# Kernel optimization log

Hardware: AMD Instinct MI355X
Metric: run time of the kernel (lower is better)

Reference implementation:

```python
import jax, jax.numpy as jnp
import numpy as np

N = 50000      # num_nodes
E = 800000     # num_edges (avg degree 16)
F_IN = 128     # num_features
H = 64         # hidden dim (fixed in module code)
C = 16         # num_classes
R = 8          # num_relations
BN_EPS = 1e-5


def setup_inputs() -> dict:
    key = jax.random.key(0)
    ks = jax.random.split(key, 16)
    s = 0.05
    f32 = jnp.float32
    inp = {
        "x": jax.random.normal(ks[0], (N, F_IN), f32),
        "edge_index": jax.random.randint(ks[1], (2, E), 0, N, dtype=jnp.int32),
        "edge_type": jax.random.randint(ks[2], (E,), 0, R, dtype=jnp.int32),
        # RGCNConv layer 1: per-relation weights, root weight, bias
        "W1": jax.random.normal(ks[3], (R, F_IN, H), f32) * s,
        "root1": jax.random.normal(ks[4], (F_IN, H), f32) * s,
        "b1": jnp.zeros((H,), f32),
        # RGCNConv layer 2
        "W2": jax.random.normal(ks[5], (R, H, H), f32) * s,
        "root2": jax.random.normal(ks[6], (H, H), f32) * s,
        "b2": jnp.zeros((H,), f32),
        # RGCNConv layer 3
        "W3": jax.random.normal(ks[7], (R, H, H), f32) * s,
        "root3": jax.random.normal(ks[8], (H, H), f32) * s,
        "b3": jnp.zeros((H,), f32),
        # BatchNorm1d params + running stats (eval mode)
        "gamma1": jnp.ones((H,), f32), "beta1": jnp.zeros((H,), f32),
        "rm1": jnp.zeros((H,), f32),   "rv1": jnp.ones((H,), f32),
        "gamma2": jnp.ones((H,), f32), "beta2": jnp.zeros((H,), f32),
        "rm2": jnp.zeros((H,), f32),   "rv2": jnp.ones((H,), f32),
        "gamma3": jnp.ones((H,), f32), "beta3": jnp.zeros((H,), f32),
        "rm3": jnp.zeros((H,), f32),   "rv3": jnp.ones((H,), f32),
        # final linear
        "Wl": jax.random.normal(ks[9], (H, C), f32) * s,
        "bl": jnp.zeros((C,), f32),
    }
    return inp


def _rgcn(x, src, dst, edge_type, W, root, bias):
    # RGCNConv with mean aggregation per relation (PyG default):
    # out_i = x_i @ root + bias + sum_r mean_{j in N_r(i)} (x_j @ W_r)
    out = x @ root + bias
    for r in range(R):  # small fixed loop over relations
        h = x @ W[r]                      # [N, H] node-level transform
        mask = (edge_type == r)
        msg = jnp.where(mask[:, None], h[src], 0.0)   # [E, H]
        agg = jax.ops.segment_sum(msg, dst, num_segments=N)   # [N, H]
        cnt = jax.ops.segment_sum(mask.astype(x.dtype), dst, num_segments=N)
        out = out + agg / jnp.maximum(cnt, 1.0)[:, None]
    return out


def _bn(x, gamma, beta, rm, rv):
    # BatchNorm1d in eval mode with running stats
    return (x - rm) * jax.lax.rsqrt(rv + BN_EPS) * gamma + beta


def reference(x, edge_index, edge_type,
              W1, root1, b1, W2, root2, b2, W3, root3, b3,
              gamma1, beta1, rm1, rv1,
              gamma2, beta2, rm2, rv2,
              gamma3, beta3, rm3, rv3,
              Wl, bl):
    src, dst = edge_index[0], edge_index[1]
    h = jax.nn.relu(_rgcn(x, src, dst, edge_type, W1, root1, b1))
    h = _bn(h, gamma1, beta1, rm1, rv1)  # dropout = identity in eval
    h = jax.nn.relu(_rgcn(h, src, dst, edge_type, W2, root2, b2))
    h = _bn(h, gamma2, beta2, rm2, rv2)
    h = jax.nn.relu(_rgcn(h, src, dst, edge_type, W3, root3, b3))
    h = _bn(h, gamma3, beta3, rm3, rv3)
    return h @ Wl + bl  # [N, C]
```

## Files before the change

kernel.cpp:

```cpp
#include <hip/hip_runtime.h>


#define R_REL 8

typedef unsigned short ushort_t;
typedef short short8 __attribute__((ext_vector_type(8)));
typedef float f32x4 __attribute__((ext_vector_type(4)));

#define MFMA(a, b, c) __builtin_amdgcn_mfma_f32_16x16x32_bf16(a, b, c, 0, 0, 0)

static __device__ __forceinline__ unsigned short f2bf(float f) {
    unsigned int u = __float_as_uint(f);
    u = (u + 0x7FFF + ((u >> 16) & 1)) >> 16;
    return (unsigned short)u;
}
static __device__ __forceinline__ float bf2f(unsigned short h) {
    return __uint_as_float(((unsigned int)h) << 16);
}

struct WcvtA {
    const float* src[6];
    ushort_t*    dst[6];
    int          end[6];
    int          K[6];
};
__global__ void wcvt6_kernel(WcvtA a, int total)
{
    int i = blockIdx.x * 256 + threadIdx.x;
    if (i >= total) return;
    int s = 0;
    while (i >= a.end[s]) ++s;
    int j = i - (s ? a.end[s - 1] : 0);
    int K = a.K[s];
    int g = j / (K * 64), rem = j % (K * 64), k = rem >> 6, c = rem & 63;
    a.dst[s][(size_t)g * 64 * K + (size_t)c * K + k] = f2bf(a.src[s][j]);
}

template<int K, bool AF32>
__global__ __launch_bounds__(256)
void mgemm_kernel(const void* __restrict__ Av, int n,
                  const ushort_t* __restrict__ WT, const ushort_t* __restrict__ RT,
                  const float* __restrict__ bias,
                  ushort_t* __restrict__ H, float* __restrict__ accb)
{
    __shared__ ushort_t As[64][136];
    __shared__ ushort_t Bs[64][136];

    const int row0 = blockIdx.x * 64;
    const int yr = blockIdx.y;
    const ushort_t* Bsrc = (yr < R_REL) ? (WT + (size_t)yr * 64 * K) : RT;

    const int tid = threadIdx.x;
    const int KB = K >> 3;

    for (int i = tid; i < 64 * KB; i += 256) {
        int r = i / KB, k8 = (i % KB) << 3;
        *(uint4*)&Bs[r][k8] = *(const uint4*)&Bsrc[(size_t)r * K + k8];
        if (AF32) {
            const float* Af = (const float*)Av;
            float4 f0 = make_float4(0.f, 0.f, 0.f, 0.f), f1 = f0;
            if (row0 + r < n) {
                f0 = *(const float4*)&Af[(size_t)(row0 + r) * K + k8];
                f1 = *(const float4*)&Af[(size_t)(row0 + r) * K + k8 + 4];
            }
            ushort_t t[8] = {f2bf(f0.x), f2bf(f0.y), f2bf(f0.z), f2bf(f0.w),
                             f2bf(f1.x), f2bf(f1.y), f2bf(f1.z), f2bf(f1.w)};
            *(uint4*)&As[r][k8] = *(const uint4*)t;
        } else {
            const ushort_t* Ab = (const ushort_t*)Av;
            uint4 av = make_uint4(0u, 0u, 0u, 0u);
            if (row0 + r < n) av = *(const uint4*)&Ab[(size_t)(row0 + r) * K + k8];
            *(uint4*)&As[r][k8] = av;
        }
    }
    __syncthreads();

    const int wid  = tid >> 6;
    const int lane = tid & 63;
    const int wr = (wid >> 1) << 5;
    const int wc = (wid & 1) << 5;
    const int fr = lane & 15;
    const int kg = (lane >> 4) << 3;

    f32x4 acc[2][2] = {};
    #pragma unroll
    for (int k0 = 0; k0 < K; k0 += 32) {
        short8 a0 = *(const short8*)&As[wr + fr     ][k0 + kg];
        short8 a1 = *(const short8*)&As[wr + 16 + fr][k0 + kg];
        short8 b0 = *(const short8*)&Bs[wc + fr     ][k0 + kg];
        short8 b1 = *(const short8*)&Bs[wc + 16 + fr][k0 + kg];
        acc[0][0] = MFMA(a0, b0, acc[0][0]);
        acc[0][1] = MFMA(a0, b1, acc[0][1]);
        acc[1][0] = MFMA(a1, b0, acc[1][0]);
        acc[1][1] = MFMA(a1, b1, acc[1][1]);
    }
    __syncthreads();

    float* Ct = (float*)As;
    const int rbase = (lane >> 4) << 2;
    #pragma unroll
    for (int m = 0; m < 2; ++m)
        #pragma unroll
        for (int nn = 0; nn < 2; ++nn)
            #pragma unroll
            for (int j = 0; j < 4; ++j)
                Ct[(wr + m * 16 + rbase + j) * 68 + wc + nn * 16 + fr] = acc[m][nn][j];
    __syncthreads();

    if (yr < R_REL) {
        const int cb = yr << 6;
        for (int i = tid; i < 64 * 8; i += 256) {
            int r = i >> 3, c8 = (i & 7) << 3;
            if (row0 + r < n) {
                ushort_t t[8];
                #pragma unroll
                for (int j = 0; j < 8; ++j) t[j] = f2bf(Ct[r * 68 + c8 + j]);
                *(uint4*)&H[(size_t)(row0 + r) * 512 + cb + c8] = *(const uint4*)t;
            }
        }
    } else {
        for (int i = tid; i < 64 * 16; i += 256) {
            int r = i >> 4, c4 = (i & 15) << 2;
            if (row0 + r < n) {
                float4 o;
                o.x = Ct[r * 68 + c4 + 0] + bias[c4 + 0];
                o.y = Ct[r * 68 + c4 + 1] + bias[c4 + 1];
                o.z = Ct[r * 68 + c4 + 2] + bias[c4 + 2];
                o.w = Ct[r * 68 + c4 + 3] + bias[c4 + 3];
                *(float4*)&accb[(size_t)(row0 + r) * 64 + c4] = o;
            }
        }
    }
}

__global__ void count_kernel(const int* __restrict__ ei, const int* __restrict__ et,
                             int* __restrict__ cnt, int E)
{
    int e = blockIdx.x * 256 + threadIdx.x;
    if (e < E) atomicAdd(&cnt[(size_t)ei[E + e] * R_REL + et[e]], 1);
}

__global__ void invdeg_scan_kernel(float* __restrict__ inv, int* __restrict__ deg,
                                   int* __restrict__ offs, int* __restrict__ partials,
                                   int N)
{
    __shared__ int sm[256];
    int i = blockIdx.x * 256 + threadIdx.x;
    int tot = 0;
    if (i < N) {
        const int* c = (const int*)inv;
        float out[R_REL];
        #pragma unroll
        for (int r = 0; r < R_REL; ++r) {
            int cc = c[(size_t)i * R_REL + r];
            tot += cc;
            out[r] = 1.0f / (float)(cc > 1 ? cc : 1);
        }
        #pragma unroll
        for (int r = 0; r < R_REL; ++r) inv[(size_t)i * R_REL + r] = out[r];
        deg[i] = tot;
    }
    sm[threadIdx.x] = tot;
    __syncthreads();
    for (int off = 1; off < 256; off <<= 1) {
        int t = (threadIdx.x >= off) ? sm[threadIdx.x - off] : 0;
        __syncthreads();
        sm[threadIdx.x] += t;
        __syncthreads();
    }
    if (i < N) offs[i] = sm[threadIdx.x] - tot;
    if (threadIdx.x == 255) partials[blockIdx.x] = sm[255];
}

__global__ void scan2_kernel(int* __restrict__ partials, int P)
{
    __shared__ int sm[256];
    __shared__ int carry;
    if (threadIdx.x == 0) carry = 0;
    __syncthreads();
    for (int base = 0; base < P; base += 256) {
        int i = base + threadIdx.x;
        int c = (i < P) ? partials[i] : 0;
        sm[threadIdx.x] = c;
        __syncthreads();
        for (int off = 1; off < 256; off <<= 1) {
            int t = (threadIdx.x >= off) ? sm[threadIdx.x - off] : 0;
            __syncthreads();
            sm[threadIdx.x] += t;
            __syncthreads();
        }
        int incl = sm[threadIdx.x];
        int cold = carry;
        if (i < P) partials[i] = incl - c + cold;
        __syncthreads();
        if (threadIdx.x == 0) carry = cold + sm[255];
        __syncthreads();
    }
}

__global__ void scan3_kernel(int* __restrict__ offs, const int* __restrict__ partials, int N)
{
    int i = blockIdx.x * 256 + threadIdx.x;
    if (i < N) offs[i] += partials[blockIdx.x];
}

__global__ void fill3_kernel(const int* __restrict__ ei, const int* __restrict__ et,
                             const int* __restrict__ offs, int* __restrict__ cursor,
                             const float* __restrict__ inv,
                             int2* __restrict__ ep, int E)
{
    int e = blockIdx.x * 256 + threadIdx.x;
    if (e >= E) return;
    int d = ei[E + e];
    int r = et[e];
    int pos = offs[d] + atomicAdd(&cursor[d], 1);
    ep[pos] = make_int2(ei[e] * 512 + r * 64,
                        __float_as_int(inv[(size_t)d * R_REL + r]));
}

__global__ __launch_bounds__(256)
void agg5_kernel(const int2* __restrict__ ep,
                 const int* __restrict__ offs, const int* __restrict__ deg,
                 const ushort_t* __restrict__ H, const float* __restrict__ accb,
                 const float* __restrict__ g, const float* __restrict__ b,
                 const float* __restrict__ rm, const float* __restrict__ rv,
                 ushort_t* __restrict__ xout,
                 const float* __restrict__ Wl, const float* __restrict__ bl,
                 float* __restrict__ out, int N, int last)
{
    const int lane = threadIdx.x & 63;
    const int d = (blockIdx.x * 256 + threadIdx.x) >> 6;
    if (d >= N) return;

    const int sub = lane >> 4;
    const int fl  = lane & 15;
    const int n0 = offs[d];
    const int dg = deg[d];

    float s0 = 0.f, s1 = 0.f, s2 = 0.f, s3 = 0.f;
    int k = 0;

    for (; k + 8 <= dg; k += 8) {
        int2 eA = ep[n0 + k + sub];
        int2 eB = ep[n0 + k + 4 + sub];
        uint2 hA = *(const uint2*)&H[(size_t)eA.x + (fl << 2)];
        uint2 hB = *(const uint2*)&H[(size_t)eB.x + (fl << 2)];
        float wA = __int_as_float(eA.y);
        float wB = __int_as_float(eB.y);
        s0 += bf2f((ushort_t)(hA.x & 0xFFFF)) * wA + bf2f((ushort_t)(hB.x & 0xFFFF)) * wB;
        s1 += bf2f((ushort_t)(hA.x >> 16))    * wA + bf2f((ushort_t)(hB.x >> 16))    * wB;
        s2 += bf2f((ushort_t)(hA.y & 0xFFFF)) * wA + bf2f((ushort_t)(hB.y & 0xFFFF)) * wB;
        s3 += bf2f((ushort_t)(hA.y >> 16))    * wA + bf2f((ushort_t)(hB.y >> 16))    * wB;
    }
    for (; k + 4 <= dg; k += 4) {
        int2 eA = ep[n0 + k + sub];
        uint2 hA = *(const uint2*)&H[(size_t)eA.x + (fl << 2)];
        float wA = __int_as_float(eA.y);
        s0 += bf2f((ushort_t)(hA.x & 0xFFFF)) * wA;
        s1 += bf2f((ushort_t)(hA.x >> 16))    * wA;
        s2 += bf2f((ushort_t)(hA.y & 0xFFFF)) * wA;
        s3 += bf2f((ushort_t)(hA.y >> 16))    * wA;
    }
    if (k < dg && sub < dg - k) {
        int2 eA = ep[n0 + k + sub];
        uint2 hA = *(const uint2*)&H[(size_t)eA.x + (fl << 2)];
        float wA = __int_as_float(eA.y);
        s0 += bf2f((ushort_t)(hA.x & 0xFFFF)) * wA;
        s1 += bf2f((ushort_t)(hA.x >> 16))    * wA;
        s2 += bf2f((ushort_t)(hA.y & 0xFFFF)) * wA;
        s3 += bf2f((ushort_t)(hA.y >> 16))    * wA;
    }

    s0 += __shfl_xor(s0, 16); s1 += __shfl_xor(s1, 16);
    s2 += __shfl_xor(s2, 16); s3 += __shfl_xor(s3, 16);
    s0 += __shfl_xor(s0, 32); s1 += __shfl_xor(s1, 32);
    s2 += __shfl_xor(s2, 32); s3 += __shfl_xor(s3, 32);

    if (sub == 0) {
        const int c4 = fl << 2;
        float4 aq = *(const float4*)&accb[(size_t)d * 64 + c4];
        float4 gm = *(const float4*)&g[c4];
        float4 bt = *(const float4*)&b[c4];
        float4 mu = *(const float4*)&rm[c4];
        float4 vr = *(const float4*)&rv[c4];
        float t0 = aq.x + s0, t1 = aq.y + s1, t2 = aq.z + s2, t3 = aq.w + s3;
        t0 = t0 > 0.f ? t0 : 0.f;  t1 = t1 > 0.f ? t1 : 0.f;
        t2 = t2 > 0.f ? t2 : 0.f;  t3 = t3 > 0.f ? t3 : 0.f;
        t0 = (t0 - mu.x) * rsqrtf(vr.x + 1e-5f) * gm.x + bt.x;
        t1 = (t1 - mu.y) * rsqrtf(vr.y + 1e-5f) * gm.y + bt.y;
        t2 = (t2 - mu.z) * rsqrtf(vr.z + 1e-5f) * gm.z + bt.z;
        t3 = (t3 - mu.w) * rsqrtf(vr.w + 1e-5f) * gm.w + bt.w;

        if (!last) {
            ushort_t o[4] = {f2bf(t0), f2bf(t1), f2bf(t2), f2bf(t3)};
            *(uint2*)&xout[(size_t)d * 64 + c4] = *(const uint2*)o;
        } else {
            f32x4 p[4] = {};
            float tt[4] = {t0, t1, t2, t3};
            #pragma unroll
            for (int i = 0; i < 4; ++i) {
                const float* wrow = &Wl[(size_t)(c4 + i) * 16];
                #pragma unroll
                for (int q = 0; q < 4; ++q)
                    p[q] += tt[i] * (*(const f32x4*)&wrow[q * 4]);
            }
            #pragma unroll
            for (int m = 1; m < 16; m <<= 1) {
                #pragma unroll
                for (int q = 0; q < 4; ++q) {
                    p[q][0] += __shfl_xor(p[q][0], m);
                    p[q][1] += __shfl_xor(p[q][1], m);
                    p[q][2] += __shfl_xor(p[q][2], m);
                    p[q][3] += __shfl_xor(p[q][3], m);
                }
            }
            if (fl == 0) {
                #pragma unroll
                for (int q = 0; q < 4; ++q) {
                    f32x4 bv = *(const f32x4*)&bl[q * 4];
                    f32x4 o = p[q] + bv;
                    *(f32x4*)&out[(size_t)d * 16 + q * 4] = o;
                }
            }
        }
    }
}

extern "C" void kernel_launch(void* const* d_in, const int* in_sizes, int n_in,
                              void* d_out, int out_size, void* d_ws, size_t ws_size,
                              hipStream_t stream)
{
    const float* x  = (const float*)d_in[0];
    const int*   ei = (const int*)d_in[1];
    const int*   et = (const int*)d_in[2];
    const float* W[3]    = {(const float*)d_in[3], (const float*)d_in[6], (const float*)d_in[9]};
    const float* root[3] = {(const float*)d_in[4], (const float*)d_in[7], (const float*)d_in[10]};
    const float* bias[3] = {(const float*)d_in[5], (const float*)d_in[8], (const float*)d_in[11]};
    const float* gamma[3] = {(const float*)d_in[12], (const float*)d_in[16], (const float*)d_in[20]};
    const float* beta[3]  = {(const float*)d_in[13], (const float*)d_in[17], (const float*)d_in[21]};
    const float* rm[3]    = {(const float*)d_in[14], (const float*)d_in[18], (const float*)d_in[22]};
    const float* rv[3]    = {(const float*)d_in[15], (const float*)d_in[19], (const float*)d_in[23]};
    const float* Wl = (const float*)d_in[24];
    const float* bl = (const float*)d_in[25];

    const int N = in_sizes[0] / 128;
    const int E = in_sizes[2];
    const int K1 = 128;

    char* p = (char*)d_ws;
    float*   inv  = (float*)p;    p += (size_t)N * R_REL * 4;
    ushort_t* Hbuf = (ushort_t*)p; p += (size_t)N * 512 * 2;
    float*   accb = (float*)p;    p += (size_t)N * 64 * 4;
    ushort_t* xb  = (ushort_t*)p; p += (size_t)N * 64 * 2;
    ushort_t* wt0 = (ushort_t*)p; p += (size_t)R_REL * 64 * K1 * 2;
    ushort_t* wt1 = (ushort_t*)p; p += (size_t)R_REL * 64 * 64 * 2;
    ushort_t* wt2 = (ushort_t*)p; p += (size_t)R_REL * 64 * 64 * 2;
    ushort_t* rt0 = (ushort_t*)p; p += (size_t)64 * K1 * 2;
    ushort_t* rt1 = (ushort_t*)p; p += (size_t)64 * 64 * 2;
    ushort_t* rt2 = (ushort_t*)p; p += (size_t)64 * 64 * 2;
    int*   offs    = (int*)p;     p += (size_t)N * 4;
    int*   deg     = (int*)p;     p += (size_t)N * 4;
    int*   cursor  = (int*)p;     p += (size_t)N * 4;
    int2*  ep      = (int2*)p;    p += (size_t)E * 8;
    int*   partials = (int*)p;

    const ushort_t* wt[3] = {wt0, wt1, wt2};
    const ushort_t* rt[3] = {rt0, rt1, rt2};

    const int gxN = (N + 255) / 256;

    {
        WcvtA a;
        a.src[0] = W[0];   a.dst[0] = wt0; a.K[0] = K1;
        a.src[1] = W[1];   a.dst[1] = wt1; a.K[1] = 64;
        a.src[2] = W[2];   a.dst[2] = wt2; a.K[2] = 64;
        a.src[3] = root[0]; a.dst[3] = rt0; a.K[3] = K1;
        a.src[4] = root[1]; a.dst[4] = rt1; a.K[4] = 64;
        a.src[5] = root[2]; a.dst[5] = rt2; a.K[5] = 64;
        int sizes[6] = {R_REL * K1 * 64, R_REL * 64 * 64, R_REL * 64 * 64,
                        K1 * 64, 64 * 64, 64 * 64};
        int acc = 0;
        for (int i = 0; i < 6; ++i) { acc += sizes[i]; a.end[i] = acc; }
        wcvt6_kernel<<<(acc + 255) / 256, 256, 0, stream>>>(a, acc);
    }

    hipMemsetAsync(inv, 0, (size_t)N * R_REL * 4, stream);
    hipMemsetAsync(cursor, 0, (size_t)N * 4, stream);
    count_kernel<<<(E + 255) / 256, 256, 0, stream>>>(ei, et, (int*)inv, E);
    invdeg_scan_kernel<<<gxN, 256, 0, stream>>>(inv, deg, offs, partials, N);
    scan2_kernel<<<1, 256, 0, stream>>>(partials, gxN);
    scan3_kernel<<<gxN, 256, 0, stream>>>(offs, partials, N);
    fill3_kernel<<<(E + 255) / 256, 256, 0, stream>>>(ei, et, offs, cursor, inv, ep, E);

    const int gx = (N + 63) / 64;
    const int gagg = (N * 64 + 255) / 256;
    const ushort_t* cur = nullptr;
    for (int layer = 0; layer < 3; ++layer) {
        if (layer == 0)
            mgemm_kernel<128, true><<<dim3(gx, R_REL + 1), 256, 0, stream>>>(
                (const void*)x, N, wt[0], rt[0], bias[0], Hbuf, accb);
        else
            mgemm_kernel<64, false><<<dim3(gx, R_REL + 1), 256, 0, stream>>>(
                (const void*)cur, N, wt[layer], rt[layer], bias[layer], Hbuf, accb);
        int last = (layer == 2);
        agg5_kernel<<<gagg, 256, 0, stream>>>(
            ep, offs, deg, Hbuf, accb,
            gamma[layer], beta[layer], rm[layer], rv[layer],
            xb, Wl, bl, (float*)d_out, N, last);
        cur = xb;
    }
}
```

Before: 413.3 us.

## Reuse A tile across three relation weights per GEMM block; split final linear

The GEMM now loads the activation tile into LDS once and loops over three weight matrices (relations or root) per block, so grid.y drops from 9 to 3 and A loads and the fp32-to-bf16 conversion are amortised. A separate C tile buffer is added in shared memory, which raises LDS use per block. The final BN-then-linear projection is moved out of the aggregation kernel into a separate lin_kernel that reads the bf16 layer output. This simplifies the aggregation kernel but adds a launch and an extra round trip of the last hidden layer through memory.

```diff
diff --git a/kernel.cpp b/kernel.cpp
--- a/kernel.cpp
+++ b/kernel.cpp
@@ -38,24 +38,21 @@
 
 template<int K, bool AF32>
 __global__ __launch_bounds__(256)
-void mgemm_kernel(const void* __restrict__ Av, int n,
-                  const ushort_t* __restrict__ WT, const ushort_t* __restrict__ RT,
-                  const float* __restrict__ bias,
-                  ushort_t* __restrict__ H, float* __restrict__ accb)
-{
-    __shared__ ushort_t As[64][136];
-    __shared__ ushort_t Bs[64][136];
+void mgemm3_kernel(const void* __restrict__ Av, int n,
+                   const ushort_t* __restrict__ WT, const ushort_t* __restrict__ RT,
+                   const float* __restrict__ bias,
+                   ushort_t* __restrict__ H, float* __restrict__ accb)
+{
+    __shared__ ushort_t As[64][K + 8];
+    __shared__ ushort_t Bs[64][K + 8];
+    __shared__ float    Ct[64][68];
 
     const int row0 = blockIdx.x * 64;
-    const int yr = blockIdx.y;
-    const ushort_t* Bsrc = (yr < R_REL) ? (WT + (size_t)yr * 64 * K) : RT;
-
     const int tid = threadIdx.x;
     const int KB = K >> 3;
 
     for (int i = tid; i < 64 * KB; i += 256) {
         int r = i / KB, k8 = (i % KB) << 3;
-        *(uint4*)&Bs[r][k8] = *(const uint4*)&Bsrc[(size_t)r * K + k8];
         if (AF32) {
             const float* Af = (const float*)Av;
             float4 f0 = make_float4(0.f, 0.f, 0.f, 0.f), f1 = f0;
@@ -73,7 +70,6 @@
             *(uint4*)&As[r][k8] = av;
         }
     }
-    __syncthreads();
 
     const int wid  = tid >> 6;
     const int lane = tid & 63;
@@ -81,53 +77,64 @@
     const int wc = (wid & 1) << 5;
     const int fr = lane & 15;
     const int kg = (lane >> 4) << 3;
-
-    f32x4 acc[2][2] = {};
-    #pragma unroll
-    for (int k0 = 0; k0 < K; k0 += 32) {
-        short8 a0 = *(const short8*)&As[wr + fr     ][k0 + kg];
-        short8 a1 = *(const short8*)&As[wr + 16 + fr][k0 + kg];
-        short8 b0 = *(const short8*)&Bs[wc + fr     ][k0 + kg];
-        short8 b1 = *(const short8*)&Bs[wc + 16 + fr][k0 + kg];
-        acc[0][0] = MFMA(a0, b0, acc[0][0]);
-        acc[0][1] = MFMA(a0, b1, acc[0][1]);
-        acc[1][0] = MFMA(a1, b0, acc[1][0]);
-        acc[1][1] = MFMA(a1, b1, acc[1][1]);
-    }
-    __syncthreads();
-
-    float* Ct = (float*)As;
     const int rbase = (lane >> 4) << 2;
-    #pragma unroll
-    for (int m = 0; m < 2; ++m)
+
+    for (int j = 0; j < 3; ++j) {
+        const int r = blockIdx.y * 3 + j;
+        const ushort_t* Bsrc = (r < R_REL) ? (WT + (size_t)r * 64 * K) : RT;
+
+        __syncthreads();
+        for (int i = tid; i < 64 * KB; i += 256) {
+            int rr = i / KB, k8 = (i % KB) << 3;
+            *(uint4*)&Bs[rr][k8] = *(const uint4*)&Bsrc[(size_t)rr * K + k8];
+        }
+        __syncthreads();
+
+        f32x4 acc[2][2] = {};
         #pragma unroll
-        for (int nn = 0; nn < 2; ++nn)
+        for (int k0 = 0; k0 < K; k0 += 32) {
+            short8 a0 = *(const short8*)&As[wr + fr     ][k0 + kg];
+            short8 a1 = *(const short8*)&As[wr + 16 + fr][k0 + kg];
+            short8 b0 = *(const short8*)&Bs[wc + fr     ][k0 + kg];
+            short8 b1 = *(const short8*)&Bs[wc + 16 + fr][k0 + kg];
+            acc[0][0] = MFMA(a0, b0, acc[0][0]);
+            acc[0][1] = MFMA(a0, b1, acc[0][1]);
+            acc[1][0] = MFMA(a1, b0, acc[1][0]);
+            acc[1][1] = MFMA(a1, b1, acc[1][1]);
+        }
+        __syncthreads();
+
+        #pragma unroll
+        for (int m = 0; m < 2; ++m)
             #pragma unroll
-            for (int j = 0; j < 4; ++j)
-                Ct[(wr + m * 16 + rbase + j) * 68 + wc + nn * 16 + fr] = acc[m][nn][j];
-    __syncthreads();
-
-    if (yr < R_REL) {
-        const int cb = yr << 6;
-        for (int i = tid; i < 64 * 8; i += 256) {
-            int r = i >> 3, c8 = (i & 7) << 3;
-            if (row0 + r < n) {
-                ushort_t t[8];
+            for (int nn = 0; nn < 2; ++nn)
                 #pragma unroll
-                for (int j = 0; j < 8; ++j) t[j] = f2bf(Ct[r * 68 + c8 + j]);
-                *(uint4*)&H[(size_t)(row0 + r) * 512 + cb + c8] = *(const uint4*)t;
+                for (int q = 0; q < 4; ++q)
+                    Ct[wr + m * 16 + rbase + q][wc + nn * 16 + fr] = acc[m][nn][q];
+        __syncthreads();
+
+        if (r < R_REL) {
+            const int cb = r << 6;
+            for (int i = tid; i < 64 * 8; i += 256) {
+                int rr = i >> 3, c8 = (i & 7) << 3;
+                if (row0 + rr < n) {
+                    ushort_t t[8];
+                    #pragma unroll
+                    for (int q = 0; q < 8; ++q) t[q] = f2bf(Ct[rr][c8 + q]);
+                    *(uint4*)&H[(size_t)(row0 + rr) * 512 + cb + c8] = *(const uint4*)t;
+                }
             }
-        }
-    } else {
-        for (int i = tid; i < 64 * 16; i += 256) {
-            int r = i >> 4, c4 = (i & 15) << 2;
-            if (row0 + r < n) {
-                float4 o;
-                o.x = Ct[r * 68 + c4 + 0] + bias[c4 + 0];
-                o.y = Ct[r * 68 + c4 + 1] + bias[c4 + 1];
-                o.z = Ct[r * 68 + c4 + 2] + bias[c4 + 2];
-                o.w = Ct[r * 68 + c4 + 3] + bias[c4 + 3];
-                *(float4*)&accb[(size_t)(row0 + r) * 64 + c4] = o;
+        } else {
+            for (int i = tid; i < 64 * 16; i += 256) {
+                int rr = i >> 4, c4 = (i & 15) << 2;
+                if (row0 + rr < n) {
+                    float4 o;
+                    o.x = Ct[rr][c4 + 0] + bias[c4 + 0];
+                    o.y = Ct[rr][c4 + 1] + bias[c4 + 1];
+                    o.z = Ct[rr][c4 + 2] + bias[c4 + 2];
+                    o.w = Ct[rr][c4 + 3] + bias[c4 + 3];
+                    *(float4*)&accb[(size_t)(row0 + rr) * 64 + c4] = o;
+                }
             }
         }
     }
@@ -219,14 +226,12 @@
 }
 
 __global__ __launch_bounds__(256)
-void agg5_kernel(const int2* __restrict__ ep,
+void agg3_kernel(const int2* __restrict__ ep,
                  const int* __restrict__ offs, const int* __restrict__ deg,
                  const ushort_t* __restrict__ H, const float* __restrict__ accb,
                  const float* __restrict__ g, const float* __restrict__ b,
                  const float* __restrict__ rm, const float* __restrict__ rv,
-                 ushort_t* __restrict__ xout,
-                 const float* __restrict__ Wl, const float* __restrict__ bl,
-                 float* __restrict__ out, int N, int last)
+                 ushort_t* __restrict__ xout, int N)
 {
     const int lane = threadIdx.x & 63;
     const int d = (blockIdx.x * 256 + threadIdx.x) >> 6;
@@ -278,52 +283,41 @@
 
     if (sub == 0) {
         const int c4 = fl << 2;
-        float4 aq = *(const float4*)&accb[(size_t)d * 64 + c4];
+        float4 a  = *(const float4*)&accb[(size_t)d * 64 + c4];
         float4 gm = *(const float4*)&g[c4];
         float4 bt = *(const float4*)&b[c4];
         float4 mu = *(const float4*)&rm[c4];
         float4 vr = *(const float4*)&rv[c4];
-        float t0 = aq.x + s0, t1 = aq.y + s1, t2 = aq.z + s2, t3 = aq.w + s3;
+        float t0 = a.x + s0, t1 = a.y + s1, t2 = a.z + s2, t3 = a.w + s3;
         t0 = t0 > 0.f ? t0 : 0.f;  t1 = t1 > 0.f ? t1 : 0.f;
         t2 = t2 > 0.f ? t2 : 0.f;  t3 = t3 > 0.f ? t3 : 0.f;
         t0 = (t0 - mu.x) * rsqrtf(vr.x + 1e-5f) * gm.x + bt.x;
         t1 = (t1 - mu.y) * rsqrtf(vr.y + 1e-5f) * gm.y + bt.y;
         t2 = (t2 - mu.z) * rsqrtf(vr.z + 1e-5f) * gm.z + bt.z;
         t3 = (t3 - mu.w) * rsqrtf(vr.w + 1e-5f) * gm.w + bt.w;
-
-        if (!last) {
-            ushort_t o[4] = {f2bf(t0), f2bf(t1), f2bf(t2), f2bf(t3)};
-            *(uint2*)&xout[(size_t)d * 64 + c4] = *(const uint2*)o;
-        } else {
-            f32x4 p[4] = {};
-            float tt[4] = {t0, t1, t2, t3};
-            #pragma unroll
-            for (int i = 0; i < 4; ++i) {
-                const float* wrow = &Wl[(size_t)(c4 + i) * 16];
-                #pragma unroll
-                for (int q = 0; q < 4; ++q)
-                    p[q] += tt[i] * (*(const f32x4*)&wrow[q * 4]);
-            }
-            #pragma unroll
-            for (int m = 1; m < 16; m <<= 1) {
-                #pragma unroll
-                for (int q = 0; q < 4; ++q) {
-                    p[q][0] += __shfl_xor(p[q][0], m);
-                    p[q][1] += __shfl_xor(p[q][1], m);
-                    p[q][2] += __shfl_xor(p[q][2], m);
-                    p[q][3] += __shfl_xor(p[q][3], m);
-                }
-            }
-            if (fl == 0) {
-                #pragma unroll
-                for (int q = 0; q < 4; ++q) {
-                    f32x4 bv = *(const f32x4*)&bl[q * 4];
-                    f32x4 o = p[q] + bv;
-                    *(f32x4*)&out[(size_t)d * 16 + q * 4] = o;
-                }
-            }
-        }
-    }
+        ushort_t o[4] = {f2bf(t0), f2bf(t1), f2bf(t2), f2bf(t3)};
+        *(uint2*)&xout[(size_t)d * 64 + c4] = *(const uint2*)o;
+    }
+}
+
+__global__ __launch_bounds__(256)
+void lin_kernel(const ushort_t* __restrict__ h, const float* __restrict__ Wl,
+                const float* __restrict__ bl, float* __restrict__ out, int N)
+{
+    __shared__ float w[64 * 16];
+    __shared__ float bb[16];
+    for (int i = threadIdx.x; i < 64 * 16; i += 256) w[i] = Wl[i];
+    if (threadIdx.x < 16) bb[threadIdx.x] = bl[threadIdx.x];
+    __syncthreads();
+
+    int idx = blockIdx.x * 256 + threadIdx.x;
+    if (idx >= N * 16) return;
+    int node = idx >> 4, c = idx & 15;
+    float s = bb[c];
+    const ushort_t* hr = h + (size_t)node * 64;
+    #pragma unroll 16
+    for (int k = 0; k < 64; ++k) s += bf2f(hr[k]) * w[k * 16 + c];
+    out[idx] = s;
 }
 
 extern "C" void kernel_launch(void* const* d_in, const int* in_sizes, int n_in,
@@ -397,16 +391,16 @@
     const ushort_t* cur = nullptr;
     for (int layer = 0; layer < 3; ++layer) {
         if (layer == 0)
-            mgemm_kernel<128, true><<<dim3(gx, R_REL + 1), 256, 0, stream>>>(
+            mgemm3_kernel<128, true><<<dim3(gx, 3), 256, 0, stream>>>(
                 (const void*)x, N, wt[0], rt[0], bias[0], Hbuf, accb);
         else
-            mgemm_kernel<64, false><<<dim3(gx, R_REL + 1), 256, 0, stream>>>(
+            mgemm3_kernel<64, false><<<dim3(gx, 3), 256, 0, stream>>>(
                 (const void*)cur, N, wt[layer], rt[layer], bias[layer], Hbuf, accb);
-        int last = (layer == 2);
-        agg5_kernel<<<gagg, 256, 0, stream>>>(
+        agg3_kernel<<<gagg, 256, 0, stream>>>(
             ep, offs, deg, Hbuf, accb,
-            gamma[layer], beta[layer], rm[layer], rv[layer],
-            xb, Wl, bl, (float*)d_out, N, last);
+            gamma[layer], beta[layer], rm[layer], rv[layer], xb, N);
         cur = xb;
     }
-}
+
+    lin_kernel<<<(N * 16 + 255) / 256, 256, 0, stream>>>(cur, Wl, bl, (float*)d_out, N);
+}
```

After: 378.5 us. 8.4% less time.
